# Kernel optimization log

Measured on AMD Instinct MI355X. Metric: run time of the kernel, lower is better.

## Reference

```python
import jax, jax.numpy as jnp
import numpy as np

B, S, D_IN, H = 64, 512, 1024, 1024


def setup_inputs() -> dict:
    key = jax.random.key(0)
    ks = jax.random.split(key, 7)
    scale = 1.0 / np.sqrt(H)  # nn.LSTM init range ~ U(-1/sqrt(H), 1/sqrt(H))
    return {
        "x": jax.random.normal(ks[0], (B, S, D_IN), dtype=jnp.float32),
        "h0": jax.random.normal(ks[1], (1, B, H), dtype=jnp.float32),
        "c0": jax.random.normal(ks[2], (1, B, H), dtype=jnp.float32),
        "w_ih": jax.random.uniform(ks[3], (4 * H, D_IN), jnp.float32, -scale, scale),
        "w_hh": jax.random.uniform(ks[4], (4 * H, H), jnp.float32, -scale, scale),
        "b_ih": jax.random.uniform(ks[5], (4 * H,), jnp.float32, -scale, scale),
        "b_hh": jax.random.uniform(ks[6], (4 * H,), jnp.float32, -scale, scale),
    }


def reference(x, h0, c0, w_ih, w_hh, b_ih, b_hh):
    # Precompute the input projection for all timesteps: [B, S, 4H]
    x_proj = jnp.einsum("bsd,nd->bsn", x, w_ih)
    bias = b_ih + b_hh  # [4H]
    hdim = w_hh.shape[1]

    def step(carry, xp_t):
        h, c = carry  # [B, H] each
        gates = xp_t + h @ w_hh.T + bias  # [B, 4H], gate order i,f,g,o
        i = jax.nn.sigmoid(gates[:, 0 * hdim:1 * hdim])
        f = jax.nn.sigmoid(gates[:, 1 * hdim:2 * hdim])
        g = jnp.tanh(gates[:, 2 * hdim:3 * hdim])
        o = jax.nn.sigmoid(gates[:, 3 * hdim:4 * hdim])
        c_next = f * c + i * g
        h_next = o * jnp.tanh(c_next)
        return (h_next, c_next), None

    (h_n, _c_n), _ = jax.lax.scan(step, (h0[0], c0[0]), jnp.swapaxes(x_proj, 0, 1))
    # num_layers == 1 -> h_n_first is empty; final hidden state stacked on layer dim
    return h_n[None]  # [1, B, H]
```

## Files before the change

### kernel.cpp

```cpp
#include <hip/hip_runtime.h>

typedef short s8v __attribute__((ext_vector_type(8)));
typedef float f4v __attribute__((ext_vector_type(4)));
typedef int   i4v __attribute__((ext_vector_type(4)));
typedef unsigned short u16;
typedef unsigned char u8;

#define CH 128
#define NCH 4
#define NRB 128

__device__ __forceinline__ u16 f2bf(float f) {
  unsigned u = __builtin_bit_cast(unsigned, f);
  u = (u + 0x7fffu + ((u >> 16) & 1u)) >> 16;
  return (u16)u;
}
__device__ __forceinline__ float bf2f(u16 h) {
  unsigned u = ((unsigned)h) << 16;
  return __builtin_bit_cast(float, u);
}
__device__ __forceinline__ int q8(float f, float s) {
  return (int)rintf(f * s);
}

__global__ void k_cast(const float* __restrict__ x, const float* __restrict__ wih,
                       const float* __restrict__ whh, const float* __restrict__ bih,
                       const float* __restrict__ bhh, const float* __restrict__ h0,
                       const float* __restrict__ c0, u16* __restrict__ xb,
                       u16* __restrict__ wihb, u8* __restrict__ whh8,
                       float* __restrict__ bias, u8* __restrict__ hbuf8,
                       float* __restrict__ cst) {
  unsigned i = blockIdx.x * 256u + threadIdx.x;
  const unsigned NT = 8192u * 256u;
  for (unsigned j = i; j < 8388608u; j += NT) {
    float4 v = ((const float4*)x)[j];
    ushort4 o; o.x = f2bf(v.x); o.y = f2bf(v.y); o.z = f2bf(v.z); o.w = f2bf(v.w);
    ((ushort4*)xb)[j] = o;
  }
  if (i < 1048576u) {
    float4 v = ((const float4*)wih)[i];
    ushort4 o; o.x = f2bf(v.x); o.y = f2bf(v.y); o.z = f2bf(v.z); o.w = f2bf(v.w);
    ((ushort4*)wihb)[i] = o;
    float4 w = ((const float4*)whh)[i];
    unsigned p = ((unsigned)(q8(w.x, 4064.f) & 255)) |
                 ((unsigned)(q8(w.y, 4064.f) & 255) << 8) |
                 ((unsigned)(q8(w.z, 4064.f) & 255) << 16) |
                 ((unsigned)(q8(w.w, 4064.f) & 255) << 24);
    ((unsigned*)whh8)[i] = p;
  }
  if (i < 16384u) {
    float4 v = ((const float4*)h0)[i];
    unsigned p = ((unsigned)(q8(v.x, 25.4f) & 255)) |
                 ((unsigned)(q8(v.y, 25.4f) & 255) << 8) |
                 ((unsigned)(q8(v.z, 25.4f) & 255) << 16) |
                 ((unsigned)(q8(v.w, 25.4f) & 255) << 24);
    ((unsigned*)hbuf8)[i] = p;
    ((float4*)cst)[i] = ((const float4*)c0)[i];
  }
  if (i < 4096u) bias[i] = bih[i] + bhh[i];
}

__device__ __forceinline__ void gemm_tile(const u16* __restrict__ xb,
                                          const u16* __restrict__ wihb,
                                          u16* __restrict__ xpl, int s0,
                                          int mt, int nt, int t, char* smem) {
  u16* lds = (u16*)smem;
  const int lane = t & 63, w = t >> 6;
  const int wm = (w >> 1) * 64, wn = (w & 1) * 64;
  const int lr = lane & 15, lk = lane >> 4;
  f4v acc[4][4] = {};
  const size_t arow0 = (size_t)(mt * 512 + s0) * 1024;
  const size_t brow0 = (size_t)(nt * 128) * 1024;
  for (int k0 = 0; k0 < 1024; k0 += 64) {
    #pragma unroll
    for (int i = 0; i < 4; i++) {
      int f16 = i * 256 + t;
      int row = f16 >> 3;
      int colb = (f16 & 7) << 4;
      int dst = row * 128 + (colb ^ ((row & 7) << 4));
      s8v va = *(const s8v*)(xb + arow0 + (size_t)row * 1024 + k0 + (colb >> 1));
      *(s8v*)((char*)lds + dst) = va;
      s8v vb = *(const s8v*)(wihb + brow0 + (size_t)row * 1024 + k0 + (colb >> 1));
      *(s8v*)((char*)lds + 16384 + dst) = vb;
    }
    __syncthreads();
    #pragma unroll
    for (int ks = 0; ks < 2; ks++) {
      s8v af[4], bf[4];
      #pragma unroll
      for (int mi = 0; mi < 4; mi++) {
        int r = wm + mi * 16 + lr;
        int cb = (ks * 64 + lk * 16) ^ ((r & 7) << 4);
        af[mi] = *(const s8v*)((const char*)lds + r * 128 + cb);
      }
      #pragma unroll
      for (int ni = 0; ni < 4; ni++) {
        int r = wn + ni * 16 + lr;
        int cb = (ks * 64 + lk * 16) ^ ((r & 7) << 4);
        bf[ni] = *(const s8v*)((const char*)lds + 16384 + r * 128 + cb);
      }
      #pragma unroll
      for (int mi = 0; mi < 4; mi++)
        #pragma unroll
        for (int ni = 0; ni < 4; ni++)
          acc[mi][ni] = __builtin_amdgcn_mfma_f32_16x16x32_bf16(af[mi], bf[ni], acc[mi][ni], 0, 0, 0);
    }
    __syncthreads();
  }
  int nioff[4];
  const int bq = mt >> 4, b15 = mt & 15;
  #pragma unroll
  for (int ni = 0; ni < 4; ni++) {
    int col = nt * 128 + wn + ni * 16 + lr;
    int gate = col >> 10, u = col & 1023;
    int gw = (u >> 3) * 4 + bq;
    int l = (b15 << 2) | ((u >> 1) & 3);
    nioff[ni] = gw * 512 + l * 8 + gate * 2 + (u & 1);
  }
  #pragma unroll
  for (int mi = 0; mi < 4; mi++)
    #pragma unroll
    for (int rr = 0; rr < 4; rr++) {
      int tloc = wm + mi * 16 + lk * 4 + rr;
      u16* dst = xpl + (size_t)tloc * 262144;
      #pragma unroll
      for (int ni = 0; ni < 4; ni++) dst[nioff[ni]] = f2bf(acc[mi][ni][rr]);
    }
}

__global__ __launch_bounds__(256, 2) void k_gemm(const u16* __restrict__ xb,
                                                 const u16* __restrict__ wihb,
                                                 u16* __restrict__ xpl, int s0) {
  __shared__ __align__(16) char smem[32768];
  const int bx = blockIdx.x;
  gemm_tile(xb, wihb, xpl, s0, bx >> 5, bx & 31, threadIdx.x, smem);
}

__device__ __forceinline__ void gbar2(unsigned* flags, unsigned ep) {
  __syncthreads();
  if (threadIdx.x < 64) {
    if (threadIdx.x == 0)
      __hip_atomic_store(flags + (size_t)blockIdx.x * 16, ep,
                         __ATOMIC_RELAXED, __HIP_MEMORY_SCOPE_AGENT);
    const int l = threadIdx.x;
    for (;;) {
      unsigned a = __hip_atomic_load(flags + l * 16,        __ATOMIC_RELAXED, __HIP_MEMORY_SCOPE_AGENT);
      unsigned b = __hip_atomic_load(flags + (l + 64) * 16, __ATOMIC_RELAXED, __HIP_MEMORY_SCOPE_AGENT);
      if (__all(a >= ep && b >= ep)) break;
    }
  }
  __syncthreads();
}

__global__ __launch_bounds__(256, 1) void k_fused(
    const u8* __restrict__ whh8, const u16* __restrict__ xpl_c,
    u16* __restrict__ xpl_n, const float* __restrict__ bias,
    float* __restrict__ cst, u8* __restrict__ hbuf8, float* __restrict__ out,
    unsigned* __restrict__ flags, const u16* __restrict__ xb,
    const u16* __restrict__ wihb, int chunk) {
  __shared__ __align__(16) char smem[32768];
  const int bid = blockIdx.x;
  const int t = threadIdx.x;
  if (bid >= NRB) {
    if (chunk + 1 < NCH) {
      const int gb = bid - NRB;
      for (int ti = 0; ti < 16; ti++) {
        int tt = gb * 16 + ti;
        gemm_tile(xb, wihb, xpl_n, (chunk + 1) * CH, tt >> 5, tt & 31, t, smem);
      }
    }
    return;
  }
  const int lane = t & 63, w = t >> 6, lr = lane & 15, lk = lane >> 4;
  long breg[2][32];
  #pragma unroll
  for (int nt = 0; nt < 2; nt++) {
    int grow = (lr >> 2) * 1024 + bid * 8 + nt * 4 + (lr & 3);
    const u8* wp = whh8 + (size_t)grow * 1024 + lk * 8;
    #pragma unroll
    for (int ks = 0; ks < 32; ks++) breg[nt][ks] = *(const long*)(wp + ks * 32);
  }
  const int me = w * 16 + (lane >> 2);
  const int u0 = bid * 8 + (lane & 3) * 2;
  const float2 bi  = *(const float2*)(bias + u0);
  const float2 bff = *(const float2*)(bias + 1024 + u0);
  const float2 bgg = *(const float2*)(bias + 2048 + u0);
  const float2 bo  = *(const float2*)(bias + 3072 + u0);
  float2 c = *(const float2*)(cst + me * 1024 + u0);
  float* glw = (float*)smem + w * (16 * 36);
  const unsigned epb = (unsigned)(chunk * CH);
  int cur = 0;
  for (int tl = 0; tl < CH; tl++) {
    s8v xq;
    asm volatile("global_load_dwordx4 %0, %1, off"
                 : "=v"(xq) : "v"(xpl_c + (size_t)tl * 262144 + (bid * 4 + w) * 512 + lane * 8) : "memory");
    const u8* ap = hbuf8 + cur * 65536 + (w * 16 + lr) * 1024 + lk * 8;
    long af[32];
    #pragma unroll
    for (int ks = 0; ks < 32; ks++)
      asm volatile("global_load_dwordx2 %0, %1, off sc0 sc1"
                   : "=v"(af[ks]) : "v"(ap + ks * 32) : "memory");
    i4v acc0 = {0, 0, 0, 0}, acc1 = {0, 0, 0, 0};
    asm volatile("s_waitcnt vmcnt(16)" ::: "memory");
    __builtin_amdgcn_sched_barrier(0);
    #pragma unroll
    for (int ks = 0; ks < 16; ks++) {
      acc0 = __builtin_amdgcn_mfma_i32_16x16x32_i8(af[ks], breg[0][ks], acc0, 0, 0, 0);
      acc1 = __builtin_amdgcn_mfma_i32_16x16x32_i8(af[ks], breg[1][ks], acc1, 0, 0, 0);
    }
    asm volatile("s_waitcnt vmcnt(0)" ::: "memory");
    __builtin_amdgcn_sched_barrier(0);
    #pragma unroll
    for (int ks = 16; ks < 32; ks++) {
      acc0 = __builtin_amdgcn_mfma_i32_16x16x32_i8(af[ks], breg[0][ks], acc0, 0, 0, 0);
      acc1 = __builtin_amdgcn_mfma_i32_16x16x32_i8(af[ks], breg[1][ks], acc1, 0, 0, 0);
    }
    const float gsc = (chunk == 0 && tl == 0) ? (5.f / (127.f * 4064.f))
                                              : (1.f / (127.f * 4064.f));
    #pragma unroll
    for (int r = 0; r < 4; r++) {
      int mrow = lk * 4 + r;
      glw[mrow * 36 + (lr & 3) * 4 + (lr >> 2)] = (float)acc0[r] * gsc;
      glw[mrow * 36 + 16 + (lr & 3) * 4 + (lr >> 2)] = (float)acc1[r] * gsc;
    }
    asm volatile("s_waitcnt lgkmcnt(0)" ::: "memory");
    __builtin_amdgcn_sched_barrier(0);
    float4 q0 = *(const float4*)(glw + (lane >> 2) * 36 + (lane & 3) * 8);
    float4 q1 = *(const float4*)(glw + (lane >> 2) * 36 + (lane & 3) * 8 + 4);
    float pi0 = q0.x + bf2f((u16)xq[0]) + bi.x;
    float pi1 = q1.x + bf2f((u16)xq[1]) + bi.y;
    float pf0 = q0.y + bf2f((u16)xq[2]) + bff.x;
    float pf1 = q1.y + bf2f((u16)xq[3]) + bff.y;
    float pg0 = q0.z + bf2f((u16)xq[4]) + bgg.x;
    float pg1 = q1.z + bf2f((u16)xq[5]) + bgg.y;
    float po0 = q0.w + bf2f((u16)xq[6]) + bo.x;
    float po1 = q1.w + bf2f((u16)xq[7]) + bo.y;
    float i0 = 1.f / (1.f + __expf(-pi0)), i1 = 1.f / (1.f + __expf(-pi1));
    float f0 = 1.f / (1.f + __expf(-pf0)), f1 = 1.f / (1.f + __expf(-pf1));
    float g0 = 1.f - 2.f / (__expf(2.f * pg0) + 1.f), g1 = 1.f - 2.f / (__expf(2.f * pg1) + 1.f);
    float o0 = 1.f / (1.f + __expf(-po0)), o1 = 1.f / (1.f + __expf(-po1));
    c.x = f0 * c.x + i0 * g0;
    c.y = f1 * c.y + i1 * g1;
    float hv0 = o0 * (1.f - 2.f / (__expf(2.f * c.x) + 1.f));
    float hv1 = o1 * (1.f - 2.f / (__expf(2.f * c.y) + 1.f));
    int nxt = cur ^ 1;
    int qh0 = (int)rintf(hv0 * 127.f), qh1 = (int)rintf(hv1 * 127.f);
    unsigned hw = ((unsigned)(qh0 & 255)) | ((unsigned)(qh1 & 255) << 8);
    asm volatile("global_store_short %0, %1, off sc0 sc1"
                 :: "v"(hbuf8 + nxt * 65536 + me * 1024 + u0), "v"(hw) : "memory");
    cur = nxt;
    if (tl < CH - 1) {
      asm volatile("s_waitcnt vmcnt(0)" ::: "memory");
      gbar2(flags, epb + (unsigned)tl + 1u);
    } else {
      if (chunk == NCH - 1) *(float2*)(out + me * 1024 + u0) = make_float2(hv0, hv1);
      else *(float2*)(cst + me * 1024 + u0) = c;
    }
  }
}

extern "C" void kernel_launch(void* const* d_in, const int* in_sizes, int n_in,
                              void* d_out, int out_size, void* d_ws, size_t ws_size,
                              hipStream_t stream) {
  const float* x   = (const float*)d_in[0];
  const float* h0  = (const float*)d_in[1];
  const float* c0  = (const float*)d_in[2];
  const float* wih = (const float*)d_in[3];
  const float* whh = (const float*)d_in[4];
  const float* bih = (const float*)d_in[5];
  const float* bhh = (const float*)d_in[6];
  float* out = (float*)d_out;
  char* ws = (char*)d_ws;
  u16* xb     = (u16*)(ws);
  u16* wihb   = (u16*)(ws + 67108864);
  u8*  whh8   = (u8*)(ws + 75497472);
  float* bias = (float*)(ws + 79691776);
  u8*  hbuf8  = (u8*)(ws + 79708160);
  float* cst  = (float*)(ws + 79839232);
  unsigned* flags = (unsigned*)(ws + 80101376);
  u16* xpl0   = (u16*)(ws + 80117760);
  u16* xpl1   = (u16*)(ws + 147226624);
  (void)in_sizes; (void)n_in; (void)out_size; (void)ws_size;

  hipMemsetAsync(flags, 0, 16384, stream);
  hipLaunchKernelGGL(k_cast, dim3(8192), dim3(256), 0, stream,
                     x, wih, whh, bih, bhh, h0, c0, xb, wihb, whh8, bias, hbuf8, cst);
  hipLaunchKernelGGL(k_gemm, dim3(2048), dim3(256), 0, stream, xb, wihb, xpl0, 0);
  for (int c = 0; c < NCH; c++) {
    u16* xc = (c & 1) ? xpl1 : xpl0;
    u16* xn = (c & 1) ? xpl0 : xpl1;
    hipLaunchKernelGGL(k_fused, dim3(256), dim3(256), 0, stream,
                       whh8, xc, xn, bias, cst, hbuf8, out, flags, xb, wihb, c);
  }
}
```

Before: 3.467 ms.

## Replace global flag barrier with epoch-tagged hidden-state packets polled by consumers

Removes the per-timestep grid-wide flag barrier. Each producer now writes its quantized hidden-state slice as a 16-byte packet with epoch tags in the first and last words. Consumers spin-load the packets until every tag matches the expected step, then run the MFMAs. This drops a full barrier round trip and the flag memset per step, but doubles the hidden-buffer traffic and relies on 16-byte stores being observed atomically.

```diff
diff --git a/kernel.cpp b/kernel.cpp
--- a/kernel.cpp
+++ b/kernel.cpp
@@ -3,6 +3,7 @@
 typedef short s8v __attribute__((ext_vector_type(8)));
 typedef float f4v __attribute__((ext_vector_type(4)));
 typedef int   i4v __attribute__((ext_vector_type(4)));
+typedef int   i2v __attribute__((ext_vector_type(2)));
 typedef unsigned short u16;
 typedef unsigned char u8;
 
@@ -19,16 +20,14 @@
   unsigned u = ((unsigned)h) << 16;
   return __builtin_bit_cast(float, u);
 }
-__device__ __forceinline__ int q8(float f, float s) {
-  return (int)rintf(f * s);
-}
+__device__ __forceinline__ int q8(float f, float s) { return (int)rintf(f * s); }
 
 __global__ void k_cast(const float* __restrict__ x, const float* __restrict__ wih,
                        const float* __restrict__ whh, const float* __restrict__ bih,
                        const float* __restrict__ bhh, const float* __restrict__ h0,
                        const float* __restrict__ c0, u16* __restrict__ xb,
                        u16* __restrict__ wihb, u8* __restrict__ whh8,
-                       float* __restrict__ bias, u8* __restrict__ hbuf8,
+                       float* __restrict__ bias, char* __restrict__ hxt,
                        float* __restrict__ cst) {
   unsigned i = blockIdx.x * 256u + threadIdx.x;
   const unsigned NT = 8192u * 256u;
@@ -48,14 +47,19 @@
                  ((unsigned)(q8(w.w, 4064.f) & 255) << 24);
     ((unsigned*)whh8)[i] = p;
   }
-  if (i < 16384u) {
-    float4 v = ((const float4*)h0)[i];
-    unsigned p = ((unsigned)(q8(v.x, 25.4f) & 255)) |
-                 ((unsigned)(q8(v.y, 25.4f) & 255) << 8) |
-                 ((unsigned)(q8(v.z, 25.4f) & 255) << 16) |
-                 ((unsigned)(q8(v.w, 25.4f) & 255) << 24);
-    ((unsigned*)hbuf8)[i] = p;
-    ((float4*)cst)[i] = ((const float4*)c0)[i];
+  if (i < 16384u) ((float4*)cst)[i] = ((const float4*)c0)[i];
+  if (i < 8192u) {
+    int row = (int)(i >> 7), g = (int)(i & 127);
+    const float* hp = h0 + row * 1024 + g * 8;
+    unsigned lo = 0, hi = 0;
+    #pragma unroll
+    for (int j = 0; j < 4; j++) lo |= (unsigned)(q8(hp[j], 25.4f) & 255) << (8 * j);
+    #pragma unroll
+    for (int j = 0; j < 4; j++) hi |= (unsigned)(q8(hp[4 + j], 25.4f) & 255) << (8 * j);
+    i4v p; p[0] = 1; p[1] = (int)lo; p[2] = (int)hi; p[3] = 1;
+    *(i4v*)(hxt + (size_t)i * 16) = p;
+    i4v z = {0, 0, 0, 0};
+    *(i4v*)(hxt + 131072 + (size_t)i * 16) = z;
   }
   if (i < 4096u) bias[i] = bih[i] + bhh[i];
 }
@@ -136,28 +140,11 @@
   gemm_tile(xb, wihb, xpl, s0, bx >> 5, bx & 31, threadIdx.x, smem);
 }
 
-__device__ __forceinline__ void gbar2(unsigned* flags, unsigned ep) {
-  __syncthreads();
-  if (threadIdx.x < 64) {
-    if (threadIdx.x == 0)
-      __hip_atomic_store(flags + (size_t)blockIdx.x * 16, ep,
-                         __ATOMIC_RELAXED, __HIP_MEMORY_SCOPE_AGENT);
-    const int l = threadIdx.x;
-    for (;;) {
-      unsigned a = __hip_atomic_load(flags + l * 16,        __ATOMIC_RELAXED, __HIP_MEMORY_SCOPE_AGENT);
-      unsigned b = __hip_atomic_load(flags + (l + 64) * 16, __ATOMIC_RELAXED, __HIP_MEMORY_SCOPE_AGENT);
-      if (__all(a >= ep && b >= ep)) break;
-    }
-  }
-  __syncthreads();
-}
-
 __global__ __launch_bounds__(256, 1) void k_fused(
     const u8* __restrict__ whh8, const u16* __restrict__ xpl_c,
     u16* __restrict__ xpl_n, const float* __restrict__ bias,
-    float* __restrict__ cst, u8* __restrict__ hbuf8, float* __restrict__ out,
-    unsigned* __restrict__ flags, const u16* __restrict__ xb,
-    const u16* __restrict__ wihb, int chunk) {
+    float* __restrict__ cst, char* __restrict__ hxt, float* __restrict__ out,
+    const u16* __restrict__ xb, const u16* __restrict__ wihb, int chunk) {
   __shared__ __align__(16) char smem[32768];
   const int bid = blockIdx.x;
   const int t = threadIdx.x;
@@ -188,32 +175,37 @@
   const float2 bo  = *(const float2*)(bias + 3072 + u0);
   float2 c = *(const float2*)(cst + me * 1024 + u0);
   float* glw = (float*)smem + w * (16 * 36);
-  const unsigned epb = (unsigned)(chunk * CH);
-  int cur = 0;
+  short* gw = (short*)(smem + 12288 + w * 128);
+  const int T0 = chunk * CH;
   for (int tl = 0; tl < CH; tl++) {
+    const int gt = T0 + tl;
     s8v xq;
     asm volatile("global_load_dwordx4 %0, %1, off"
                  : "=v"(xq) : "v"(xpl_c + (size_t)tl * 262144 + (bid * 4 + w) * 512 + lane * 8) : "memory");
-    const u8* ap = hbuf8 + cur * 65536 + (w * 16 + lr) * 1024 + lk * 8;
-    long af[32];
-    #pragma unroll
-    for (int ks = 0; ks < 32; ks++)
-      asm volatile("global_load_dwordx2 %0, %1, off sc0 sc1"
-                   : "=v"(af[ks]) : "v"(ap + ks * 32) : "memory");
+    const char* ap = hxt + (size_t)(gt & 1) * 131072 + (w * 16 + lr) * 2048 + lk * 16;
+    const int e = gt + 1;
+    i4v q[32];
+    for (;;) {
+      #pragma unroll
+      for (int ks = 0; ks < 32; ks++)
+        asm volatile("global_load_dwordx4 %0, %1, off sc0 sc1"
+                     : "=v"(q[ks]) : "v"(ap + ks * 64) : "memory");
+      asm volatile("s_waitcnt vmcnt(0)" ::: "memory");
+      __builtin_amdgcn_sched_barrier(0);
+      int ok = 1;
+      #pragma unroll
+      for (int ks = 0; ks < 32; ks++) ok &= (q[ks][0] >= e) & (q[ks][3] >= e);
+      if (__all(ok)) break;
+      __builtin_amdgcn_s_sleep(1);
+    }
+    __builtin_amdgcn_sched_barrier(0);
     i4v acc0 = {0, 0, 0, 0}, acc1 = {0, 0, 0, 0};
-    asm volatile("s_waitcnt vmcnt(16)" ::: "memory");
-    __builtin_amdgcn_sched_barrier(0);
-    #pragma unroll
-    for (int ks = 0; ks < 16; ks++) {
-      acc0 = __builtin_amdgcn_mfma_i32_16x16x32_i8(af[ks], breg[0][ks], acc0, 0, 0, 0);
-      acc1 = __builtin_amdgcn_mfma_i32_16x16x32_i8(af[ks], breg[1][ks], acc1, 0, 0, 0);
-    }
-    asm volatile("s_waitcnt vmcnt(0)" ::: "memory");
-    __builtin_amdgcn_sched_barrier(0);
-    #pragma unroll
-    for (int ks = 16; ks < 32; ks++) {
-      acc0 = __builtin_amdgcn_mfma_i32_16x16x32_i8(af[ks], breg[0][ks], acc0, 0, 0, 0);
-      acc1 = __builtin_amdgcn_mfma_i32_16x16x32_i8(af[ks], breg[1][ks], acc1, 0, 0, 0);
+    #pragma unroll
+    for (int ks = 0; ks < 32; ks++) {
+      i2v d; d[0] = q[ks][1]; d[1] = q[ks][2];
+      long a = __builtin_bit_cast(long, d);
+      acc0 = __builtin_amdgcn_mfma_i32_16x16x32_i8(a, breg[0][ks], acc0, 0, 0, 0);
+      acc1 = __builtin_amdgcn_mfma_i32_16x16x32_i8(a, breg[1][ks], acc1, 0, 0, 0);
     }
     const float gsc = (chunk == 0 && tl == 0) ? (5.f / (127.f * 4064.f))
                                               : (1.f / (127.f * 4064.f));
@@ -243,16 +235,21 @@
     c.y = f1 * c.y + i1 * g1;
     float hv0 = o0 * (1.f - 2.f / (__expf(2.f * c.x) + 1.f));
     float hv1 = o1 * (1.f - 2.f / (__expf(2.f * c.y) + 1.f));
-    int nxt = cur ^ 1;
-    int qh0 = (int)rintf(hv0 * 127.f), qh1 = (int)rintf(hv1 * 127.f);
-    unsigned hw = ((unsigned)(qh0 & 255)) | ((unsigned)(qh1 & 255) << 8);
-    asm volatile("global_store_short %0, %1, off sc0 sc1"
-                 :: "v"(hbuf8 + nxt * 65536 + me * 1024 + u0), "v"(hw) : "memory");
-    cur = nxt;
-    if (tl < CH - 1) {
-      asm volatile("s_waitcnt vmcnt(0)" ::: "memory");
-      gbar2(flags, epb + (unsigned)tl + 1u);
-    } else {
+    if (!(chunk == NCH - 1 && tl == CH - 1)) {
+      int qh0 = (int)rintf(hv0 * 127.f), qh1 = (int)rintf(hv1 * 127.f);
+      gw[lane] = (short)((qh0 & 255) | ((qh1 & 255) << 8));
+      asm volatile("s_waitcnt lgkmcnt(0)" ::: "memory");
+      __builtin_amdgcn_sched_barrier(0);
+      if ((lane & 3) == 0) {
+        unsigned dlo = *(const unsigned*)(gw + lane);
+        unsigned dhi = *(const unsigned*)(gw + lane + 2);
+        i4v pkt; pkt[0] = gt + 2; pkt[1] = (int)dlo; pkt[2] = (int)dhi; pkt[3] = gt + 2;
+        char* dst = hxt + (size_t)((gt + 1) & 1) * 131072 + me * 2048 + bid * 16;
+        asm volatile("global_store_dwordx4 %0, %1, off sc0 sc1"
+                     :: "v"(dst), "v"(pkt) : "memory");
+      }
+    }
+    if (tl == CH - 1) {
       if (chunk == NCH - 1) *(float2*)(out + me * 1024 + u0) = make_float2(hv0, hv1);
       else *(float2*)(cst + me * 1024 + u0) = c;
     }
@@ -275,21 +272,19 @@
   u16* wihb   = (u16*)(ws + 67108864);
   u8*  whh8   = (u8*)(ws + 75497472);
   float* bias = (float*)(ws + 79691776);
-  u8*  hbuf8  = (u8*)(ws + 79708160);
-  float* cst  = (float*)(ws + 79839232);
-  unsigned* flags = (unsigned*)(ws + 80101376);
-  u16* xpl0   = (u16*)(ws + 80117760);
-  u16* xpl1   = (u16*)(ws + 147226624);
+  char* hxt   = (ws + 79708160);
+  float* cst  = (float*)(ws + 79970304);
+  u16* xpl0   = (u16*)(ws + 80232448);
+  u16* xpl1   = (u16*)(ws + 147341312);
   (void)in_sizes; (void)n_in; (void)out_size; (void)ws_size;
 
-  hipMemsetAsync(flags, 0, 16384, stream);
   hipLaunchKernelGGL(k_cast, dim3(8192), dim3(256), 0, stream,
-                     x, wih, whh, bih, bhh, h0, c0, xb, wihb, whh8, bias, hbuf8, cst);
+                     x, wih, whh, bih, bhh, h0, c0, xb, wihb, whh8, bias, hxt, cst);
   hipLaunchKernelGGL(k_gemm, dim3(2048), dim3(256), 0, stream, xb, wihb, xpl0, 0);
   for (int c = 0; c < NCH; c++) {
     u16* xc = (c & 1) ? xpl1 : xpl0;
     u16* xn = (c & 1) ? xpl0 : xpl1;
     hipLaunchKernelGGL(k_fused, dim3(256), dim3(256), 0, stream,
-                       whh8, xc, xn, bias, cst, hbuf8, out, flags, xb, wihb, c);
-  }
-}
+                       whh8, xc, xn, bias, cst, hxt, out, xb, wihb, c);
+  }
+}
```

Result: slower. 5.580 ms (+60.9%).
